# Performance work log

Hardware: AMD Instinct MI355X
Metric: run time of the kernel (lower is better)

Reference implementation:

```python
import jax, jax.numpy as jnp
import numpy as np

N_NODES = 50000
N_EDGES = 800000
IN_F, HID, OUT_F = 128, 128, 64


def setup_inputs() -> dict:
    key = jax.random.key(0)
    k1, k2, k3, k4 = jax.random.split(key, 4)
    x = jax.random.normal(k1, (N_NODES, IN_F), dtype=jnp.float32)
    edge_index = jax.random.randint(k2, (2, N_EDGES), 0, N_NODES, dtype=jnp.int64)
    # Glorot-style scaled weights, zero bias (PyG GCNConv default)
    W1 = jax.random.normal(k3, (IN_F, HID), dtype=jnp.float32) * (1.0 / np.sqrt(IN_F))
    b1 = jnp.zeros((HID,), dtype=jnp.float32)
    W2 = jax.random.normal(k4, (HID, OUT_F), dtype=jnp.float32) * (1.0 / np.sqrt(HID))
    b2 = jnp.zeros((OUT_F,), dtype=jnp.float32)
    return {"x": x, "edge_index": edge_index, "W1": W1, "b1": b1, "W2": W2, "b2": b2}


def reference(x, edge_index, W1, b1, W2, b2):
    n = x.shape[0]
    # add self-loops (PyG GCNConv default add_self_loops=True)
    loop = jnp.arange(n, dtype=edge_index.dtype)
    src = jnp.concatenate([edge_index[0], loop])  # message source nodes
    dst = jnp.concatenate([edge_index[1], loop])  # aggregation target nodes
    # symmetric normalization: D^{-1/2} (A+I) D^{-1/2}
    deg = jax.ops.segment_sum(jnp.ones(dst.shape, dtype=x.dtype), dst, num_segments=n)
    dinv = jnp.where(deg > 0, jax.lax.rsqrt(deg), 0.0)
    norm = dinv[src] * dinv[dst]  # [E+N]

    def gcn_conv(h, W, b):
        h = h @ W                              # dense transform first (PyG order)
        msg = h[src] * norm[:, None]           # gather + scale: [E+N, d]
        agg = jax.ops.segment_sum(msg, dst, num_segments=n)  # scatter-add
        return agg + b

    h = jax.nn.relu(gcn_conv(x, W1, b1))
    return gcn_conv(h, W2, b2)
```

## Files before the change

### kernel.cpp

```cpp
#include <hip/hip_runtime.h>
#include <hip/hip_bf16.h>

#define NN   50000
#define NE   800000
#define F_IN 128
#define F_H  128
#define F_O  64

#define BINSHIFT 7
#define NBINS    ((NN + 127) >> 7)
#define CAP      2816
#define EPB      8192

static constexpr int NB_G1  = (NN + 63) / 64;
static constexpr int NB_BIN = (NE + EPB - 1) / EPB;
static constexpr int NB_NODE = (NN + 255) / 256;

typedef __bf16 bf16_8 __attribute__((ext_vector_type(8)));
typedef float  f32x4  __attribute__((ext_vector_type(4)));

template <typename AT, int K, int NOUT, bool SCALE>
__device__ __forceinline__ void gemm_body(const AT* __restrict__ X,
                                          const float* __restrict__ W,
                                          const float* __restrict__ dinv,
                                          __hip_bfloat16* __restrict__ Y,
                                          __hip_bfloat16* WB, int blk) {
    constexpr int NKS = K / 32;
    constexpr int NC  = NOUT / 16;
    const int t = threadIdx.x;
    for (int f = t; f < K * NOUT; f += 256) {
        int k = f / NOUT, n = f % NOUT;
        int ks = k >> 5, kr = k & 31, qq = kr >> 3, jj = kr & 7;
        int c = n >> 4, nn = n & 15;
        WB[(((ks * NC + c) * 4 + qq) * 16 + nn) * 8 + jj] = __float2bfloat16(W[f]);
    }
    __syncthreads();

    const int wave = t >> 6, lane = t & 63;
    const int r = lane & 15, q = lane >> 4;
    const int m0 = blk * 64 + wave * 16;
    int arow = m0 + r;
    if (arow >= NN) arow = NN - 1;

    f32x4 acc[NC];
#pragma unroll
    for (int c = 0; c < NC; ++c) acc[c] = (f32x4){0.f, 0.f, 0.f, 0.f};

#pragma unroll
    for (int ks = 0; ks < NKS; ++ks) {
        bf16_8 a;
        if constexpr (sizeof(AT) == 4) {
            const float* xp = (const float*)X + (size_t)arow * K + ks * 32 + q * 8;
            float4 x0 = ((const float4*)xp)[0];
            float4 x1 = ((const float4*)xp)[1];
            a[0] = (__bf16)x0.x; a[1] = (__bf16)x0.y; a[2] = (__bf16)x0.z; a[3] = (__bf16)x0.w;
            a[4] = (__bf16)x1.x; a[5] = (__bf16)x1.y; a[6] = (__bf16)x1.z; a[7] = (__bf16)x1.w;
        } else {
            a = *(const bf16_8*)((const __hip_bfloat16*)X + (size_t)arow * K + ks * 32 + q * 8);
        }
#pragma unroll
        for (int c = 0; c < NC; ++c) {
            bf16_8 b = *(const bf16_8*)&WB[(((ks * NC + c) * 4 + q) * 16 + r) * 8];
            acc[c] = __builtin_amdgcn_mfma_f32_16x16x32_bf16(a, b, acc[c], 0, 0, 0);
        }
    }

#pragma unroll
    for (int c = 0; c < NC; ++c) {
#pragma unroll
        for (int i = 0; i < 4; ++i) {
            int gr = m0 + q * 4 + i;
            if (gr < NN) {
                float v = acc[c][i];
                if constexpr (SCALE) v *= dinv[gr];
                Y[(size_t)gr * NOUT + c * 16 + r] = __float2bfloat16(v);
            }
        }
    }
}

__global__ __launch_bounds__(256) void k_fuseA(const float* __restrict__ X,
                                               const float* __restrict__ W1,
                                               __hip_bfloat16* __restrict__ Xw,
                                               const int* __restrict__ ei32,
                                               int* __restrict__ binbuf,
                                               unsigned* __restrict__ bincnt) {
    __shared__ __align__(16) char smem[32768];
    const int t = threadIdx.x;

    if (blockIdx.x >= NB_BIN) {
        gemm_body<float, F_IN, F_H, false>(X, W1, nullptr, Xw,
                                           (__hip_bfloat16*)smem,
                                           blockIdx.x - NB_BIN);
        return;
    }

    unsigned* hist = (unsigned*)smem;
    unsigned* base = hist + NBINS;
    unsigned* rank = base + NBINS;
    for (int i = t; i < NBINS; i += 256) { hist[i] = 0u; rank[i] = 0u; }
    __syncthreads();

    const bool is64 = ((ei32[1] | ei32[3] | ei32[5] | ei32[7]) == 0);
    const long long* p64 = (const long long*)ei32;
    const int e0 = blockIdx.x * EPB;
    const int e1 = (e0 + EPB < NE) ? e0 + EPB : NE;

    for (int e = e0 + t; e < e1; e += 256) {
        int d = is64 ? (int)p64[NE + e] : ei32[NE + e];
        atomicAdd(&hist[d >> BINSHIFT], 1u);
    }
    __syncthreads();
    for (int b = t; b < NBINS; b += 256)
        base[b] = atomicAdd(&bincnt[b], hist[b]);
    __syncthreads();
    for (int e = e0 + t; e < e1; e += 256) {
        int s, d;
        if (is64) { s = (int)p64[e]; d = (int)p64[NE + e]; }
        else      { s = ei32[e];     d = ei32[NE + e]; }
        int b = d >> BINSHIFT;
        unsigned rk = atomicAdd(&rank[b], 1u);
        binbuf[(size_t)b * CAP + base[b] + rk] = (s << BINSHIFT) | (d & 127);
    }
}

__global__ __launch_bounds__(256) void k_phaseB(const int* __restrict__ binbuf,
                                                const unsigned* __restrict__ bincnt,
                                                unsigned* __restrict__ row_ptr,
                                                float* __restrict__ dinv,
                                                int* __restrict__ srcs) {
    __shared__ unsigned h[128];
    __shared__ unsigned cur[128];
    __shared__ unsigned red[256];
    const int b = blockIdx.x, t = threadIdx.x;

    unsigned part = 0;
    for (int i = t; i < NBINS; i += 256)
        if (i < b) part += bincnt[i];
    red[t] = part;
    if (t < 128) h[t] = 0u;
    __syncthreads();
    for (int off = 128; off > 0; off >>= 1) {
        if (t < off) red[t] += red[t + off];
        __syncthreads();
    }
    const unsigned gbase = red[0];

    const unsigned n = bincnt[b];
    const int* buf = binbuf + (size_t)b * CAP;
    for (unsigned i = t; i < n; i += 256)
        atomicAdd(&h[buf[i] & 127], 1u);
    __syncthreads();
    if (t < 128) cur[t] = h[t];
    __syncthreads();
    for (int off = 1; off < 128; off <<= 1) {
        unsigned u = (t < 128 && t >= off) ? cur[t - off] : 0u;
        __syncthreads();
        if (t < 128) cur[t] += u;
        __syncthreads();
    }
    if (t < 128) {
        unsigned ex = gbase + cur[t] - h[t];
        int node = (b << BINSHIFT) + t;
        if (node < NN) {
            row_ptr[node] = ex;
            dinv[node]    = rsqrtf((float)(h[t] + 1u));
        }
        cur[t] = ex;
    }
    if (b == NBINS - 1 && t == 0) row_ptr[NN] = NE;
    __syncthreads();
    for (unsigned i = t; i < n; i += 256) {
        int p = buf[i];
        unsigned pos = atomicAdd(&cur[p & 127], 1u);
        srcs[pos] = p >> BINSHIFT;
    }
}

__global__ __launch_bounds__(256) void k_agg1(const __hip_bfloat16* __restrict__ Xw,
                                              const int* __restrict__ srcs,
                                              const unsigned* __restrict__ row_ptr,
                                              const float* __restrict__ dinv,
                                              const float* __restrict__ b1,
                                              __hip_bfloat16* __restrict__ H) {
    const int wv   = (blockIdx.x * 256 + threadIdx.x) >> 6;
    const int lane = threadIdx.x & 63;
    if (wv >= NN) return;
    const int sub = lane >> 4;
    const int fl  = lane & 15;
    const float dn = dinv[wv];

    float acc0[8], acc1[8];
    bf16_8 self = *(const bf16_8*)(Xw + (size_t)wv * F_H + fl * 8);
    const float sw = (sub == 0) ? dn : 0.f;
#pragma unroll
    for (int j = 0; j < 8; ++j) { acc0[j] = sw * (float)self[j]; acc1[j] = 0.f; }

    const unsigned ie = row_ptr[wv + 1];
    unsigned i = row_ptr[wv] + sub;
    for (; i + 4 < ie; i += 8) {
        int s0 = srcs[i], s1 = srcs[i + 4];
        float d0 = dinv[s0], d1 = dinv[s1];
        bf16_8 r0 = *(const bf16_8*)(Xw + (size_t)s0 * F_H + fl * 8);
        bf16_8 r1 = *(const bf16_8*)(Xw + (size_t)s1 * F_H + fl * 8);
#pragma unroll
        for (int j = 0; j < 8; ++j) {
            acc0[j] += d0 * (float)r0[j];
            acc1[j] += d1 * (float)r1[j];
        }
    }
    if (i < ie) {
        int s = srcs[i];
        float d = dinv[s];
        bf16_8 r = *(const bf16_8*)(Xw + (size_t)s * F_H + fl * 8);
#pragma unroll
        for (int j = 0; j < 8; ++j) acc0[j] += d * (float)r[j];
    }
#pragma unroll
    for (int j = 0; j < 8; ++j) {
        float a = acc0[j] + acc1[j];
        a += __shfl_xor(a, 16, 64);
        a += __shfl_xor(a, 32, 64);
        acc0[j] = a;
    }
    if (sub == 0) {
        bf16_8 o;
#pragma unroll
        for (int j = 0; j < 8; ++j) {
            float v = fmaxf(dn * acc0[j] + b1[fl * 8 + j], 0.f);
            o[j] = (__bf16)v;
        }
        *(bf16_8*)(H + (size_t)wv * F_H + fl * 8) = o;
    }
}

__global__ __launch_bounds__(256) void k_gemm2(const __hip_bfloat16* __restrict__ H1,
                                               const float* __restrict__ W2,
                                               const float* __restrict__ dinv,
                                               __hip_bfloat16* __restrict__ Hw) {
    __shared__ __align__(16) __hip_bfloat16 WB[(F_H / 32) * (F_O / 16) * 512];
    gemm_body<__hip_bfloat16, F_H, F_O, true>(H1, W2, dinv, Hw, WB, blockIdx.x);
}

__global__ __launch_bounds__(256) void k_agg2(const __hip_bfloat16* __restrict__ Hw,
                                              const int* __restrict__ srcs,
                                              const unsigned* __restrict__ row_ptr,
                                              const float* __restrict__ dinv,
                                              const float* __restrict__ b2,
                                              float* __restrict__ out) {
    const int wv   = (blockIdx.x * 256 + threadIdx.x) >> 6;
    const int lane = threadIdx.x & 63;
    if (wv >= NN) return;
    const int sub = lane >> 3;
    const int fl  = lane & 7;

    float acc0[8], acc1[8];
    bf16_8 self = *(const bf16_8*)(Hw + (size_t)wv * F_O + fl * 8);
#pragma unroll
    for (int j = 0; j < 8; ++j) {
        acc0[j] = (sub == 0) ? (float)self[j] : 0.f;
        acc1[j] = 0.f;
    }

    const unsigned ie = row_ptr[wv + 1];
    unsigned i = row_ptr[wv] + sub;
    for (; i + 8 < ie; i += 16) {
        int s0 = srcs[i], s1 = srcs[i + 8];
        bf16_8 r0 = *(const bf16_8*)(Hw + (size_t)s0 * F_O + fl * 8);
        bf16_8 r1 = *(const bf16_8*)(Hw + (size_t)s1 * F_O + fl * 8);
#pragma unroll
        for (int j = 0; j < 8; ++j) {
            acc0[j] += (float)r0[j];
            acc1[j] += (float)r1[j];
        }
    }
    if (i < ie) {
        int s = srcs[i];
        bf16_8 r = *(const bf16_8*)(Hw + (size_t)s * F_O + fl * 8);
#pragma unroll
        for (int j = 0; j < 8; ++j) acc0[j] += (float)r[j];
    }
#pragma unroll
    for (int j = 0; j < 8; ++j) {
        float a = acc0[j] + acc1[j];
        a += __shfl_xor(a, 8, 64);
        a += __shfl_xor(a, 16, 64);
        a += __shfl_xor(a, 32, 64);
        acc0[j] = a;
    }
    if (sub == 0) {
        float dn = dinv[wv];
        float4 o0 = make_float4(dn * acc0[0] + b2[fl * 8 + 0], dn * acc0[1] + b2[fl * 8 + 1],
                                dn * acc0[2] + b2[fl * 8 + 2], dn * acc0[3] + b2[fl * 8 + 3]);
        float4 o1 = make_float4(dn * acc0[4] + b2[fl * 8 + 4], dn * acc0[5] + b2[fl * 8 + 5],
                                dn * acc0[6] + b2[fl * 8 + 6], dn * acc0[7] + b2[fl * 8 + 7]);
        float4* op = (float4*)(out + (size_t)wv * F_O + fl * 8);
        op[0] = o0;
        op[1] = o1;
    }
}

extern "C" void kernel_launch(void* const* d_in, const int* in_sizes, int n_in,
                              void* d_out, int out_size, void* d_ws, size_t ws_size,
                              hipStream_t stream) {
    const float* x  = (const float*)d_in[0];
    const int*   ei = (const int*)d_in[1];
    const float* W1 = (const float*)d_in[2];
    const float* b1 = (const float*)d_in[3];
    const float* W2 = (const float*)d_in[4];
    const float* b2 = (const float*)d_in[5];
    float* out = (float*)d_out;

    char* w = (char*)d_ws;
    size_t off = 0;
    auto alloc = [&](size_t bytes) {
        void* p = w + off;
        off += (bytes + 255) & ~(size_t)255;
        return p;
    };
    unsigned* row_ptr = (unsigned*)alloc((size_t)(NN + 1) * 4);
    float*    dinv    = (float*)alloc((size_t)NN * 4);
    unsigned* bincnt  = (unsigned*)alloc((size_t)NBINS * 4);
    int*      srcs    = (int*)alloc((size_t)NE * 4);
    int*      binbuf  = (int*)alloc((size_t)NBINS * CAP * 4);
    __hip_bfloat16* Xw = (__hip_bfloat16*)alloc((size_t)NN * F_H * 2);
    __hip_bfloat16* H1 = (__hip_bfloat16*)alloc((size_t)NN * F_H * 2);
    __hip_bfloat16* Hw = Xw;

    hipMemsetAsync(bincnt, 0, (size_t)NBINS * 4, stream);
    k_fuseA<<<NB_BIN + NB_G1, 256, 0, stream>>>(x, W1, Xw, ei, binbuf, bincnt);
    k_phaseB<<<NBINS, 256, 0, stream>>>(binbuf, bincnt, row_ptr, dinv, srcs);

    k_agg1<<<(NN + 3) / 4, 256, 0, stream>>>(Xw, srcs, row_ptr, dinv, b1, H1);
    k_gemm2<<<(NN + 63) / 64, 256, 0, stream>>>(H1, W2, dinv, Hw);
    k_agg2<<<(NN + 3) / 4, 256, 0, stream>>>(Hw, srcs, row_ptr, dinv, b2, out);
}
```

Before: 186.7 us.

## Slice feature tables into 32-column planes and prescale by dinv in phaseB

The GEMM outputs are written in a sliced layout of 32-column planes, so each aggregation block gathers 64-byte rows from a single plane. The aim is a smaller working set per pass that stays in cache, at the cost of launching one block per slice. The per-edge dinv[src] gather in agg1 is removed by prescaling Xw rows by dinv inside phaseB. GEMM blocks now cover 256 rows each, amortising the LDS weight staging over more rows. The trade-off is that the graph is traversed four times (agg1) and twice (agg2), with more srcs reads and an extra read-modify-write of Xw.

```diff
diff --git a/kernel.cpp b/kernel.cpp
--- a/kernel.cpp
+++ b/kernel.cpp
@@ -11,20 +11,20 @@
 #define NBINS    ((NN + 127) >> 7)
 #define CAP      2816
 #define EPB      8192
-
-static constexpr int NB_G1  = (NN + 63) / 64;
+#define NBW      12500
+
+static constexpr int NB_G1  = (NN + 255) / 256;
 static constexpr int NB_BIN = (NE + EPB - 1) / EPB;
-static constexpr int NB_NODE = (NN + 255) / 256;
 
 typedef __bf16 bf16_8 __attribute__((ext_vector_type(8)));
 typedef float  f32x4  __attribute__((ext_vector_type(4)));
 
-template <typename AT, int K, int NOUT, bool SCALE>
-__device__ __forceinline__ void gemm_body(const AT* __restrict__ X,
-                                          const float* __restrict__ W,
-                                          const float* __restrict__ dinv,
-                                          __hip_bfloat16* __restrict__ Y,
-                                          __hip_bfloat16* WB, int blk) {
+template <typename AT, int K, int NOUT, bool SCALE, bool SLICED>
+__device__ __forceinline__ void gemm_body256(const AT* __restrict__ X,
+                                             const float* __restrict__ W,
+                                             const float* __restrict__ dinv,
+                                             __hip_bfloat16* __restrict__ Y,
+                                             __hip_bfloat16* WB, int blk) {
     constexpr int NKS = K / 32;
     constexpr int NC  = NOUT / 16;
     const int t = threadIdx.x;
@@ -38,42 +38,50 @@
 
     const int wave = t >> 6, lane = t & 63;
     const int r = lane & 15, q = lane >> 4;
-    const int m0 = blk * 64 + wave * 16;
-    int arow = m0 + r;
-    if (arow >= NN) arow = NN - 1;
-
-    f32x4 acc[NC];
-#pragma unroll
-    for (int c = 0; c < NC; ++c) acc[c] = (f32x4){0.f, 0.f, 0.f, 0.f};
-
-#pragma unroll
-    for (int ks = 0; ks < NKS; ++ks) {
-        bf16_8 a;
-        if constexpr (sizeof(AT) == 4) {
-            const float* xp = (const float*)X + (size_t)arow * K + ks * 32 + q * 8;
-            float4 x0 = ((const float4*)xp)[0];
-            float4 x1 = ((const float4*)xp)[1];
-            a[0] = (__bf16)x0.x; a[1] = (__bf16)x0.y; a[2] = (__bf16)x0.z; a[3] = (__bf16)x0.w;
-            a[4] = (__bf16)x1.x; a[5] = (__bf16)x1.y; a[6] = (__bf16)x1.z; a[7] = (__bf16)x1.w;
-        } else {
-            a = *(const bf16_8*)((const __hip_bfloat16*)X + (size_t)arow * K + ks * 32 + q * 8);
-        }
+
+    for (int g = 0; g < 4; ++g) {
+        const int m0 = blk * 256 + g * 64 + wave * 16;
+        int arow = m0 + r;
+        if (arow >= NN) arow = NN - 1;
+
+        f32x4 acc[NC];
+#pragma unroll
+        for (int c = 0; c < NC; ++c) acc[c] = (f32x4){0.f, 0.f, 0.f, 0.f};
+
+#pragma unroll
+        for (int ks = 0; ks < NKS; ++ks) {
+            bf16_8 a;
+            if constexpr (sizeof(AT) == 4) {
+                const float* xp = (const float*)X + (size_t)arow * K + ks * 32 + q * 8;
+                float4 x0 = ((const float4*)xp)[0];
+                float4 x1 = ((const float4*)xp)[1];
+                a[0] = (__bf16)x0.x; a[1] = (__bf16)x0.y; a[2] = (__bf16)x0.z; a[3] = (__bf16)x0.w;
+                a[4] = (__bf16)x1.x; a[5] = (__bf16)x1.y; a[6] = (__bf16)x1.z; a[7] = (__bf16)x1.w;
+            } else {
+                a = *(const bf16_8*)((const __hip_bfloat16*)X + (size_t)arow * K + ks * 32 + q * 8);
+            }
+#pragma unroll
+            for (int c = 0; c < NC; ++c) {
+                bf16_8 b = *(const bf16_8*)&WB[(((ks * NC + c) * 4 + q) * 16 + r) * 8];
+                acc[c] = __builtin_amdgcn_mfma_f32_16x16x32_bf16(a, b, acc[c], 0, 0, 0);
+            }
+        }
+
 #pragma unroll
         for (int c = 0; c < NC; ++c) {
-            bf16_8 b = *(const bf16_8*)&WB[(((ks * NC + c) * 4 + q) * 16 + r) * 8];
-            acc[c] = __builtin_amdgcn_mfma_f32_16x16x32_bf16(a, b, acc[c], 0, 0, 0);
-        }
-    }
-
-#pragma unroll
-    for (int c = 0; c < NC; ++c) {
-#pragma unroll
-        for (int i = 0; i < 4; ++i) {
-            int gr = m0 + q * 4 + i;
-            if (gr < NN) {
-                float v = acc[c][i];
-                if constexpr (SCALE) v *= dinv[gr];
-                Y[(size_t)gr * NOUT + c * 16 + r] = __float2bfloat16(v);
+#pragma unroll
+            for (int i = 0; i < 4; ++i) {
+                int gr = m0 + q * 4 + i;
+                if (gr < NN) {
+                    float v = acc[c][i];
+                    if constexpr (SCALE) v *= dinv[gr];
+                    size_t yo;
+                    if constexpr (SLICED)
+                        yo = (size_t)(c >> 1) * NN * 32 + (size_t)gr * 32 + (c & 1) * 16 + r;
+                    else
+                        yo = (size_t)gr * NOUT + c * 16 + r;
+                    Y[yo] = __float2bfloat16(v);
+                }
             }
         }
     }
@@ -89,9 +97,9 @@
     const int t = threadIdx.x;
 
     if (blockIdx.x >= NB_BIN) {
-        gemm_body<float, F_IN, F_H, false>(X, W1, nullptr, Xw,
-                                           (__hip_bfloat16*)smem,
-                                           blockIdx.x - NB_BIN);
+        gemm_body256<float, F_IN, F_H, false, true>(X, W1, nullptr, Xw,
+                                                    (__hip_bfloat16*)smem,
+                                                    blockIdx.x - NB_BIN);
         return;
     }
 
@@ -128,9 +136,11 @@
                                                 const unsigned* __restrict__ bincnt,
                                                 unsigned* __restrict__ row_ptr,
                                                 float* __restrict__ dinv,
-                                                int* __restrict__ srcs) {
+                                                int* __restrict__ srcs,
+                                                __hip_bfloat16* __restrict__ Xw) {
     __shared__ unsigned h[128];
     __shared__ unsigned cur[128];
+    __shared__ float    dv[128];
     __shared__ unsigned red[256];
     const int b = blockIdx.x, t = threadIdx.x;
 
@@ -162,9 +172,11 @@
     if (t < 128) {
         unsigned ex = gbase + cur[t] - h[t];
         int node = (b << BINSHIFT) + t;
+        float d = rsqrtf((float)(h[t] + 1u));
+        dv[t] = d;
         if (node < NN) {
             row_ptr[node] = ex;
-            dinv[node]    = rsqrtf((float)(h[t] + 1u));
+            dinv[node]    = d;
         }
         cur[t] = ex;
     }
@@ -174,6 +186,21 @@
         int p = buf[i];
         unsigned pos = atomicAdd(&cur[p & 127], 1u);
         srcs[pos] = p >> BINSHIFT;
+    }
+
+    for (int idx = t; idx < 128 * 16; idx += 256) {
+        int nl = idx >> 4, ch = idx & 15;
+        int node = (b << BINSHIFT) + nl;
+        if (node < NN) {
+            int sl = ch >> 2, cc = ch & 3;
+            __hip_bfloat16* p = Xw + (size_t)sl * NN * 32 + (size_t)node * 32 + cc * 8;
+            bf16_8 v = *(const bf16_8*)p;
+            float d = dv[nl];
+            bf16_8 o;
+#pragma unroll
+            for (int j = 0; j < 8; ++j) o[j] = (__bf16)(d * (float)v[j]);
+            *(bf16_8*)p = o;
+        }
     }
 }
 
@@ -183,54 +210,55 @@
                                               const float* __restrict__ dinv,
                                               const float* __restrict__ b1,
                                               __hip_bfloat16* __restrict__ H) {
-    const int wv   = (blockIdx.x * 256 + threadIdx.x) >> 6;
-    const int lane = threadIdx.x & 63;
+    const int wave = threadIdx.x >> 6, lane = threadIdx.x & 63;
+    const int sl = blockIdx.x / NBW;
+    const int wv = (blockIdx.x % NBW) * 4 + wave;
     if (wv >= NN) return;
-    const int sub = lane >> 4;
-    const int fl  = lane & 15;
-    const float dn = dinv[wv];
+    const int fl = lane & 3, sub = lane >> 2;
+    const __hip_bfloat16* Xs = Xw + (size_t)sl * NN * 32;
 
     float acc0[8], acc1[8];
-    bf16_8 self = *(const bf16_8*)(Xw + (size_t)wv * F_H + fl * 8);
-    const float sw = (sub == 0) ? dn : 0.f;
-#pragma unroll
-    for (int j = 0; j < 8; ++j) { acc0[j] = sw * (float)self[j]; acc1[j] = 0.f; }
-
-    const unsigned ie = row_ptr[wv + 1];
+    {
+        bf16_8 r = *(const bf16_8*)(Xs + (size_t)wv * 32 + fl * 8);
+#pragma unroll
+        for (int j = 0; j < 8; ++j) {
+            acc0[j] = (sub == 0) ? (float)r[j] : 0.f;
+            acc1[j] = 0.f;
+        }
+    }
+    const unsigned i1 = row_ptr[wv + 1];
     unsigned i = row_ptr[wv] + sub;
-    for (; i + 4 < ie; i += 8) {
-        int s0 = srcs[i], s1 = srcs[i + 4];
-        float d0 = dinv[s0], d1 = dinv[s1];
-        bf16_8 r0 = *(const bf16_8*)(Xw + (size_t)s0 * F_H + fl * 8);
-        bf16_8 r1 = *(const bf16_8*)(Xw + (size_t)s1 * F_H + fl * 8);
+    for (; i + 16 < i1; i += 32) {
+        int s0 = srcs[i], s1 = srcs[i + 16];
+        bf16_8 r0 = *(const bf16_8*)(Xs + (size_t)s0 * 32 + fl * 8);
+        bf16_8 r1 = *(const bf16_8*)(Xs + (size_t)s1 * 32 + fl * 8);
 #pragma unroll
         for (int j = 0; j < 8; ++j) {
-            acc0[j] += d0 * (float)r0[j];
-            acc1[j] += d1 * (float)r1[j];
-        }
-    }
-    if (i < ie) {
-        int s = srcs[i];
-        float d = dinv[s];
-        bf16_8 r = *(const bf16_8*)(Xw + (size_t)s * F_H + fl * 8);
-#pragma unroll
-        for (int j = 0; j < 8; ++j) acc0[j] += d * (float)r[j];
+            acc0[j] += (float)r0[j];
+            acc1[j] += (float)r1[j];
+        }
+    }
+    if (i < i1) {
+        bf16_8 r = *(const bf16_8*)(Xs + (size_t)srcs[i] * 32 + fl * 8);
+#pragma unroll
+        for (int j = 0; j < 8; ++j) acc0[j] += (float)r[j];
     }
 #pragma unroll
     for (int j = 0; j < 8; ++j) {
         float a = acc0[j] + acc1[j];
+        a += __shfl_xor(a, 4, 64);
+        a += __shfl_xor(a, 8, 64);
         a += __shfl_xor(a, 16, 64);
         a += __shfl_xor(a, 32, 64);
         acc0[j] = a;
     }
     if (sub == 0) {
+        float dn = dinv[wv];
         bf16_8 o;
 #pragma unroll
-        for (int j = 0; j < 8; ++j) {
-            float v = fmaxf(dn * acc0[j] + b1[fl * 8 + j], 0.f);
-            o[j] = (__bf16)v;
-        }
-        *(bf16_8*)(H + (size_t)wv * F_H + fl * 8) = o;
+        for (int j = 0; j < 8; ++j)
+            o[j] = (__bf16)fmaxf(dn * acc0[j] + b1[sl * 32 + fl * 8 + j], 0.f);
+        *(bf16_8*)(H + (size_t)wv * F_H + sl * 32 + fl * 8) = o;
     }
 }
 
@@ -238,8 +266,8 @@
                                                const float* __restrict__ W2,
                                                const float* __restrict__ dinv,
                                                __hip_bfloat16* __restrict__ Hw) {
-    __shared__ __align__(16) __hip_bfloat16 WB[(F_H / 32) * (F_O / 16) * 512];
-    gemm_body<__hip_bfloat16, F_H, F_O, true>(H1, W2, dinv, Hw, WB, blockIdx.x);
+    __shared__ __align__(16) __hip_bfloat16 WB[F_H * F_O];
+    gemm_body256<__hip_bfloat16, F_H, F_O, true, true>(H1, W2, dinv, Hw, WB, blockIdx.x);
 }
 
 __global__ __launch_bounds__(256) void k_agg2(const __hip_bfloat16* __restrict__ Hw,
@@ -248,41 +276,43 @@
                                               const float* __restrict__ dinv,
                                               const float* __restrict__ b2,
                                               float* __restrict__ out) {
-    const int wv   = (blockIdx.x * 256 + threadIdx.x) >> 6;
-    const int lane = threadIdx.x & 63;
+    const int wave = threadIdx.x >> 6, lane = threadIdx.x & 63;
+    const int sl = blockIdx.x / NBW;
+    const int wv = (blockIdx.x % NBW) * 4 + wave;
     if (wv >= NN) return;
-    const int sub = lane >> 3;
-    const int fl  = lane & 7;
+    const int fl = lane & 3, sub = lane >> 2;
+    const __hip_bfloat16* Hs = Hw + (size_t)sl * NN * 32;
 
     float acc0[8], acc1[8];
-    bf16_8 self = *(const bf16_8*)(Hw + (size_t)wv * F_O + fl * 8);
-#pragma unroll
-    for (int j = 0; j < 8; ++j) {
-        acc0[j] = (sub == 0) ? (float)self[j] : 0.f;
-        acc1[j] = 0.f;
-    }
-
-    const unsigned ie = row_ptr[wv + 1];
+    {
+        bf16_8 r = *(const bf16_8*)(Hs + (size_t)wv * 32 + fl * 8);
+#pragma unroll
+        for (int j = 0; j < 8; ++j) {
+            acc0[j] = (sub == 0) ? (float)r[j] : 0.f;
+            acc1[j] = 0.f;
+        }
+    }
+    const unsigned i1 = row_ptr[wv + 1];
     unsigned i = row_ptr[wv] + sub;
-    for (; i + 8 < ie; i += 16) {
-        int s0 = srcs[i], s1 = srcs[i + 8];
-        bf16_8 r0 = *(const bf16_8*)(Hw + (size_t)s0 * F_O + fl * 8);
-        bf16_8 r1 = *(const bf16_8*)(Hw + (size_t)s1 * F_O + fl * 8);
+    for (; i + 16 < i1; i += 32) {
+        int s0 = srcs[i], s1 = srcs[i + 16];
+        bf16_8 r0 = *(const bf16_8*)(Hs + (size_t)s0 * 32 + fl * 8);
+        bf16_8 r1 = *(const bf16_8*)(Hs + (size_t)s1 * 32 + fl * 8);
 #pragma unroll
         for (int j = 0; j < 8; ++j) {
             acc0[j] += (float)r0[j];
             acc1[j] += (float)r1[j];
         }
     }
-    if (i < ie) {
-        int s = srcs[i];
-        bf16_8 r = *(const bf16_8*)(Hw + (size_t)s * F_O + fl * 8);
+    if (i < i1) {
+        bf16_8 r = *(const bf16_8*)(Hs + (size_t)srcs[i] * 32 + fl * 8);
 #pragma unroll
         for (int j = 0; j < 8; ++j) acc0[j] += (float)r[j];
     }
 #pragma unroll
     for (int j = 0; j < 8; ++j) {
         float a = acc0[j] + acc1[j];
+        a += __shfl_xor(a, 4, 64);
         a += __shfl_xor(a, 8, 64);
         a += __shfl_xor(a, 16, 64);
         a += __shfl_xor(a, 32, 64);
@@ -290,11 +320,15 @@
     }
     if (sub == 0) {
         float dn = dinv[wv];
-        float4 o0 = make_float4(dn * acc0[0] + b2[fl * 8 + 0], dn * acc0[1] + b2[fl * 8 + 1],
-                                dn * acc0[2] + b2[fl * 8 + 2], dn * acc0[3] + b2[fl * 8 + 3]);
-        float4 o1 = make_float4(dn * acc0[4] + b2[fl * 8 + 4], dn * acc0[5] + b2[fl * 8 + 5],
-                                dn * acc0[6] + b2[fl * 8 + 6], dn * acc0[7] + b2[fl * 8 + 7]);
-        float4* op = (float4*)(out + (size_t)wv * F_O + fl * 8);
+        float4 o0 = make_float4(dn * acc0[0] + b2[sl * 32 + fl * 8 + 0],
+                                dn * acc0[1] + b2[sl * 32 + fl * 8 + 1],
+                                dn * acc0[2] + b2[sl * 32 + fl * 8 + 2],
+                                dn * acc0[3] + b2[sl * 32 + fl * 8 + 3]);
+        float4 o1 = make_float4(dn * acc0[4] + b2[sl * 32 + fl * 8 + 4],
+                                dn * acc0[5] + b2[sl * 32 + fl * 8 + 5],
+                                dn * acc0[6] + b2[sl * 32 + fl * 8 + 6],
+                                dn * acc0[7] + b2[sl * 32 + fl * 8 + 7]);
+        float4* op = (float4*)(out + (size_t)wv * F_O + sl * 32 + fl * 8);
         op[0] = o0;
         op[1] = o1;
     }
@@ -329,9 +363,9 @@
 
     hipMemsetAsync(bincnt, 0, (size_t)NBINS * 4, stream);
     k_fuseA<<<NB_BIN + NB_G1, 256, 0, stream>>>(x, W1, Xw, ei, binbuf, bincnt);
-    k_phaseB<<<NBINS, 256, 0, stream>>>(binbuf, bincnt, row_ptr, dinv, srcs);
-
-    k_agg1<<<(NN + 3) / 4, 256, 0, stream>>>(Xw, srcs, row_ptr, dinv, b1, H1);
-    k_gemm2<<<(NN + 63) / 64, 256, 0, stream>>>(H1, W2, dinv, Hw);
-    k_agg2<<<(NN + 3) / 4, 256, 0, stream>>>(Hw, srcs, row_ptr, dinv, b2, out);
-}
+    k_phaseB<<<NBINS, 256, 0, stream>>>(binbuf, bincnt, row_ptr, dinv, srcs, Xw);
+
+    k_agg1<<<4 * NBW, 256, 0, stream>>>(Xw, srcs, row_ptr, dinv, b1, H1);
+    k_gemm2<<<NB_G1, 256, 0, stream>>>(H1, W2, dinv, Hw);
+    k_agg2<<<2 * NBW, 256, 0, stream>>>(Hw, srcs, row_ptr, dinv, b2, out);
+}
```

New measurement: 251.7 us. 1.35x slower.

## Prescale Xw by dinv in phaseB and process 256 rows per GEMM block

Applied to the files above, without the earlier changes.

Each GEMM block now covers 256 rows in four 64-row groups, so the bf16 weight staging in shared memory is spread over more work, and all A fragments of a row are loaded before the MFMAs. The source-side dinv scaling for layer 1 moves into k_phaseB, which rescales its bin's 128 Xw rows in place, so k_agg1 no longer does a dependent dinv[src] gather per edge. The cost is an extra read-modify-write pass over Xw, a second bf16 rounding of Xw, and four times fewer GEMM blocks.

```diff
diff --git a/kernel.cpp b/kernel.cpp
--- a/kernel.cpp
+++ b/kernel.cpp
@@ -12,19 +12,18 @@
 #define CAP      2816
 #define EPB      8192
 
-static constexpr int NB_G1  = (NN + 63) / 64;
+static constexpr int NB_G1  = (NN + 255) / 256;
 static constexpr int NB_BIN = (NE + EPB - 1) / EPB;
-static constexpr int NB_NODE = (NN + 255) / 256;
 
 typedef __bf16 bf16_8 __attribute__((ext_vector_type(8)));
 typedef float  f32x4  __attribute__((ext_vector_type(4)));
 
 template <typename AT, int K, int NOUT, bool SCALE>
-__device__ __forceinline__ void gemm_body(const AT* __restrict__ X,
-                                          const float* __restrict__ W,
-                                          const float* __restrict__ dinv,
-                                          __hip_bfloat16* __restrict__ Y,
-                                          __hip_bfloat16* WB, int blk) {
+__device__ __forceinline__ void gemm_body256(const AT* __restrict__ X,
+                                             const float* __restrict__ W,
+                                             const float* __restrict__ dinv,
+                                             __hip_bfloat16* __restrict__ Y,
+                                             __hip_bfloat16* WB, int blk) {
     constexpr int NKS = K / 32;
     constexpr int NC  = NOUT / 16;
     const int t = threadIdx.x;
@@ -38,42 +37,58 @@
 
     const int wave = t >> 6, lane = t & 63;
     const int r = lane & 15, q = lane >> 4;
-    const int m0 = blk * 64 + wave * 16;
-    int arow = m0 + r;
-    if (arow >= NN) arow = NN - 1;
-
-    f32x4 acc[NC];
-#pragma unroll
-    for (int c = 0; c < NC; ++c) acc[c] = (f32x4){0.f, 0.f, 0.f, 0.f};
-
-#pragma unroll
-    for (int ks = 0; ks < NKS; ++ks) {
-        bf16_8 a;
+
+    for (int g = 0; g < 4; ++g) {
+        const int m0 = blk * 256 + g * 64 + wave * 16;
+        int arow = m0 + r;
+        if (arow >= NN) arow = NN - 1;
+
+        bf16_8 afrag[NKS];
         if constexpr (sizeof(AT) == 4) {
-            const float* xp = (const float*)X + (size_t)arow * K + ks * 32 + q * 8;
-            float4 x0 = ((const float4*)xp)[0];
-            float4 x1 = ((const float4*)xp)[1];
-            a[0] = (__bf16)x0.x; a[1] = (__bf16)x0.y; a[2] = (__bf16)x0.z; a[3] = (__bf16)x0.w;
-            a[4] = (__bf16)x1.x; a[5] = (__bf16)x1.y; a[6] = (__bf16)x1.z; a[7] = (__bf16)x1.w;
+            float4 xa[NKS * 2];
+            const float4* xp = (const float4*)((const float*)X + (size_t)arow * K);
+#pragma unroll
+            for (int ks = 0; ks < NKS; ++ks) {
+                xa[ks * 2]     = xp[ks * 8 + q * 2];
+                xa[ks * 2 + 1] = xp[ks * 8 + q * 2 + 1];
+            }
+#pragma unroll
+            for (int ks = 0; ks < NKS; ++ks) {
+                float4 x0 = xa[ks * 2], x1 = xa[ks * 2 + 1];
+                afrag[ks][0] = (__bf16)x0.x; afrag[ks][1] = (__bf16)x0.y;
+                afrag[ks][2] = (__bf16)x0.z; afrag[ks][3] = (__bf16)x0.w;
+                afrag[ks][4] = (__bf16)x1.x; afrag[ks][5] = (__bf16)x1.y;
+                afrag[ks][6] = (__bf16)x1.z; afrag[ks][7] = (__bf16)x1.w;
+            }
         } else {
-            a = *(const bf16_8*)((const __hip_bfloat16*)X + (size_t)arow * K + ks * 32 + q * 8);
-        }
+            const __hip_bfloat16* xp = (const __hip_bfloat16*)X + (size_t)arow * K;
+#pragma unroll
+            for (int ks = 0; ks < NKS; ++ks)
+                afrag[ks] = *(const bf16_8*)(xp + ks * 32 + q * 8);
+        }
+
+        f32x4 acc[NC];
+#pragma unroll
+        for (int c = 0; c < NC; ++c) acc[c] = (f32x4){0.f, 0.f, 0.f, 0.f};
+#pragma unroll
+        for (int ks = 0; ks < NKS; ++ks) {
+#pragma unroll
+            for (int c = 0; c < NC; ++c) {
+                bf16_8 b = *(const bf16_8*)&WB[(((ks * NC + c) * 4 + q) * 16 + r) * 8];
+                acc[c] = __builtin_amdgcn_mfma_f32_16x16x32_bf16(afrag[ks], b, acc[c], 0, 0, 0);
+            }
+        }
+
 #pragma unroll
         for (int c = 0; c < NC; ++c) {
-            bf16_8 b = *(const bf16_8*)&WB[(((ks * NC + c) * 4 + q) * 16 + r) * 8];
-            acc[c] = __builtin_amdgcn_mfma_f32_16x16x32_bf16(a, b, acc[c], 0, 0, 0);
-        }
-    }
-
-#pragma unroll
-    for (int c = 0; c < NC; ++c) {
-#pragma unroll
-        for (int i = 0; i < 4; ++i) {
-            int gr = m0 + q * 4 + i;
-            if (gr < NN) {
-                float v = acc[c][i];
-                if constexpr (SCALE) v *= dinv[gr];
-                Y[(size_t)gr * NOUT + c * 16 + r] = __float2bfloat16(v);
+#pragma unroll
+            for (int i = 0; i < 4; ++i) {
+                int gr = m0 + q * 4 + i;
+                if (gr < NN) {
+                    float v = acc[c][i];
+                    if constexpr (SCALE) v *= dinv[gr];
+                    Y[(size_t)gr * NOUT + c * 16 + r] = __float2bfloat16(v);
+                }
             }
         }
     }
@@ -89,9 +104,9 @@
     const int t = threadIdx.x;
 
     if (blockIdx.x >= NB_BIN) {
-        gemm_body<float, F_IN, F_H, false>(X, W1, nullptr, Xw,
-                                           (__hip_bfloat16*)smem,
-                                           blockIdx.x - NB_BIN);
+        gemm_body256<float, F_IN, F_H, false>(X, W1, nullptr, Xw,
+                                              (__hip_bfloat16*)smem,
+                                              blockIdx.x - NB_BIN);
         return;
     }
 
@@ -128,9 +143,11 @@
                                                 const unsigned* __restrict__ bincnt,
                                                 unsigned* __restrict__ row_ptr,
                                                 float* __restrict__ dinv,
-                                                int* __restrict__ srcs) {
+                                                int* __restrict__ srcs,
+                                                __hip_bfloat16* __restrict__ Xw) {
     __shared__ unsigned h[128];
     __shared__ unsigned cur[128];
+    __shared__ float    dv[128];
     __shared__ unsigned red[256];
     const int b = blockIdx.x, t = threadIdx.x;
 
@@ -162,9 +179,11 @@
     if (t < 128) {
         unsigned ex = gbase + cur[t] - h[t];
         int node = (b << BINSHIFT) + t;
+        float d = rsqrtf((float)(h[t] + 1u));
+        dv[t] = d;
         if (node < NN) {
             row_ptr[node] = ex;
-            dinv[node]    = rsqrtf((float)(h[t] + 1u));
+            dinv[node]    = d;
         }
         cur[t] = ex;
     }
@@ -174,6 +193,20 @@
         int p = buf[i];
         unsigned pos = atomicAdd(&cur[p & 127], 1u);
         srcs[pos] = p >> BINSHIFT;
+    }
+
+    for (int idx = t; idx < 128 * 16; idx += 256) {
+        int nl = idx >> 4, ch = idx & 15;
+        int node = (b << BINSHIFT) + nl;
+        if (node < NN) {
+            __hip_bfloat16* p = Xw + (size_t)node * F_H + ch * 8;
+            bf16_8 v = *(const bf16_8*)p;
+            float d = dv[nl];
+            bf16_8 o;
+#pragma unroll
+            for (int j = 0; j < 8; ++j) o[j] = (__bf16)(d * (float)v[j]);
+            *(bf16_8*)p = o;
+        }
     }
 }
 
@@ -188,33 +221,31 @@
     if (wv >= NN) return;
     const int sub = lane >> 4;
     const int fl  = lane & 15;
-    const float dn = dinv[wv];
 
     float acc0[8], acc1[8];
     bf16_8 self = *(const bf16_8*)(Xw + (size_t)wv * F_H + fl * 8);
-    const float sw = (sub == 0) ? dn : 0.f;
-#pragma unroll
-    for (int j = 0; j < 8; ++j) { acc0[j] = sw * (float)self[j]; acc1[j] = 0.f; }
+#pragma unroll
+    for (int j = 0; j < 8; ++j) {
+        acc0[j] = (sub == 0) ? (float)self[j] : 0.f;
+        acc1[j] = 0.f;
+    }
 
     const unsigned ie = row_ptr[wv + 1];
     unsigned i = row_ptr[wv] + sub;
     for (; i + 4 < ie; i += 8) {
         int s0 = srcs[i], s1 = srcs[i + 4];
-        float d0 = dinv[s0], d1 = dinv[s1];
         bf16_8 r0 = *(const bf16_8*)(Xw + (size_t)s0 * F_H + fl * 8);
         bf16_8 r1 = *(const bf16_8*)(Xw + (size_t)s1 * F_H + fl * 8);
 #pragma unroll
         for (int j = 0; j < 8; ++j) {
-            acc0[j] += d0 * (float)r0[j];
-            acc1[j] += d1 * (float)r1[j];
+            acc0[j] += (float)r0[j];
+            acc1[j] += (float)r1[j];
         }
     }
     if (i < ie) {
-        int s = srcs[i];
-        float d = dinv[s];
-        bf16_8 r = *(const bf16_8*)(Xw + (size_t)s * F_H + fl * 8);
-#pragma unroll
-        for (int j = 0; j < 8; ++j) acc0[j] += d * (float)r[j];
+        bf16_8 r = *(const bf16_8*)(Xw + (size_t)srcs[i] * F_H + fl * 8);
+#pragma unroll
+        for (int j = 0; j < 8; ++j) acc0[j] += (float)r[j];
     }
 #pragma unroll
     for (int j = 0; j < 8; ++j) {
@@ -224,6 +255,7 @@
         acc0[j] = a;
     }
     if (sub == 0) {
+        float dn = dinv[wv];
         bf16_8 o;
 #pragma unroll
         for (int j = 0; j < 8; ++j) {
@@ -238,8 +270,8 @@
                                                const float* __restrict__ W2,
                                                const float* __restrict__ dinv,
                                                __hip_bfloat16* __restrict__ Hw) {
-    __shared__ __align__(16) __hip_bfloat16 WB[(F_H / 32) * (F_O / 16) * 512];
-    gemm_body<__hip_bfloat16, F_H, F_O, true>(H1, W2, dinv, Hw, WB, blockIdx.x);
+    __shared__ __align__(16) __hip_bfloat16 WB[F_H * F_O];
+    gemm_body256<__hip_bfloat16, F_H, F_O, true>(H1, W2, dinv, Hw, WB, blockIdx.x);
 }
 
 __global__ __launch_bounds__(256) void k_agg2(const __hip_bfloat16* __restrict__ Hw,
@@ -275,8 +307,7 @@
         }
     }
     if (i < ie) {
-        int s = srcs[i];
-        bf16_8 r = *(const bf16_8*)(Hw + (size_t)s * F_O + fl * 8);
+        bf16_8 r = *(const bf16_8*)(Hw + (size_t)srcs[i] * F_O + fl * 8);
 #pragma unroll
         for (int j = 0; j < 8; ++j) acc0[j] += (float)r[j];
     }
@@ -329,9 +360,9 @@
 
     hipMemsetAsync(bincnt, 0, (size_t)NBINS * 4, stream);
     k_fuseA<<<NB_BIN + NB_G1, 256, 0, stream>>>(x, W1, Xw, ei, binbuf, bincnt);
-    k_phaseB<<<NBINS, 256, 0, stream>>>(binbuf, bincnt, row_ptr, dinv, srcs);
+    k_phaseB<<<NBINS, 256, 0, stream>>>(binbuf, bincnt, row_ptr, dinv, srcs, Xw);
 
     k_agg1<<<(NN + 3) / 4, 256, 0, stream>>>(Xw, srcs, row_ptr, dinv, b1, H1);
-    k_gemm2<<<(NN + 63) / 64, 256, 0, stream>>>(H1, W2, dinv, Hw);
+    k_gemm2<<<NB_G1, 256, 0, stream>>>(H1, W2, dinv, Hw);
     k_agg2<<<(NN + 3) / 4, 256, 0, stream>>>(Hw, srcs, row_ptr, dinv, b2, out);
 }
```

After: 192.5 us. +3.1%, slower.
